# Optimization experiments

Hardware: AMD Instinct MI355X
Metric: run time of the kernel (lower is better)

Reference implementation:

```python
import jax, jax.numpy as jnp
import numpy as np

N_NODES = 100000
N_EDGES = 1600000
F_IN, F_HID, F_OUT = 64, 64, 32


def setup_inputs() -> dict:
    key = jax.random.key(0)
    k1, k2, k3, k4 = jax.random.split(key, 4)
    x = jax.random.normal(k1, (N_NODES, F_IN), dtype=jnp.float32)
    edge_idx = jax.random.randint(k2, (2, N_EDGES), 0, N_NODES, dtype=jnp.int64)
    W1 = jax.random.normal(k3, (F_IN, F_HID), dtype=jnp.float32) * (1.0 / np.sqrt(F_IN))
    b1 = jnp.zeros((F_HID,), dtype=jnp.float32)
    W2 = jax.random.normal(k4, (F_HID, F_OUT), dtype=jnp.float32) * (1.0 / np.sqrt(F_HID))
    b2 = jnp.zeros((F_OUT,), dtype=jnp.float32)
    return {"x": x, "edge_idx": edge_idx, "W1": W1, "b1": b1, "W2": W2, "b2": b2}


def _gcn_conv(h, src, dst, norm, W, b, n):
    # PyG GCNConv: transform first, then normalized sum aggregation, then bias.
    h = h @ W                                   # [N, F_out]
    msg = h[src] * norm[:, None]                # [E+N, F_out] gather + scale
    agg = jax.ops.segment_sum(msg, dst, num_segments=n)  # scatter-add
    return agg + b


def reference(x, edge_idx, W1, b1, W2, b2):
    n = x.shape[0]
    loop = jnp.arange(n, dtype=edge_idx.dtype)
    src = jnp.concatenate([edge_idx[0], loop])  # add self-loops
    dst = jnp.concatenate([edge_idx[1], loop])
    # symmetric normalization D^-1/2 (A+I) D^-1/2
    deg = jax.ops.segment_sum(jnp.ones_like(dst, dtype=x.dtype), dst, num_segments=n)
    dinv = jnp.where(deg > 0, jax.lax.rsqrt(deg), 0.0)
    norm = dinv[src] * dinv[dst]                # [E+N]

    h = _gcn_conv(x, src, dst, norm, W1, b1, n)
    h = jax.nn.relu(h)
    # dropout(p=0.5) is identity in eval mode (deterministic reference)
    out = _gcn_conv(h, src, dst, norm, W2, b2, n)
    return out
```

## Files before the change

### kernel.cpp

```cpp
#include <hip/hip_runtime.h>
#include <hip/hip_bf16.h>
#include <hip/hip_fp16.h>


#define N_FEAT_IN 64
#define B2SHIFT 9
#define CHUNK 4096
#define CAP 12288
#define CSRCAP 20480

struct alignas(8) half4 { __half2 lo, hi; };
struct alignas(16) half8 { __half2 h[4]; };

__global__ __launch_bounds__(256) void init_k(int* __restrict__ gcur) {
    gcur[threadIdx.x] = 0;
}

__global__ __launch_bounds__(1024) void place_k(const int* __restrict__ src,
                                                const int* __restrict__ dst,
                                                int* __restrict__ gcur,
                                                unsigned* __restrict__ bedges, int E) {
    __shared__ int h[256];
    __shared__ int cur[256];
    int t = threadIdx.x;
    if (t < 256) h[t] = 0;
    __syncthreads();
    int base = blockIdx.x * CHUNK;
    int end = min(base + CHUNK, E);
    for (int i = base + t; i < end; i += 1024)
        atomicAdd(&h[dst[i] >> B2SHIFT], 1);
    __syncthreads();
    if (t < 256) {
        int cnt = h[t];
        int b0 = cnt ? atomicAdd(&gcur[t], cnt) : 0;
        cur[t] = t * CAP + b0;
    }
    __syncthreads();
    for (int i = base + t; i < end; i += 1024) {
        int d = dst[i];
        int p = atomicAdd(&cur[d >> B2SHIFT], 1);
        bedges[p] = ((unsigned)src[i] << B2SHIFT) | (unsigned)(d & 511);
    }
}

__global__ __launch_bounds__(1024) void bucket_csr(const int* __restrict__ gcnt,
                                                   const unsigned* __restrict__ bedges,
                                                   int* __restrict__ row_ptr,
                                                   int* __restrict__ rend,
                                                   float* __restrict__ dinv,
                                                   int* __restrict__ csr_src, int n) {
    __shared__ int lh[512];
    __shared__ int cur[512];
    int t = threadIdx.x;
    if (t < 512) lh[t] = 0;
    __syncthreads();
    int b = blockIdx.x;
    int beg = b * CAP;
    int end = beg + gcnt[b];
    for (int i = beg + t; i < end; i += 1024)
        atomicAdd(&lh[bedges[i] & 511], 1);
    __syncthreads();
    int c = (t < 512) ? lh[t] : 0;
    __syncthreads();
    int cp = (c + 15) & ~15;
    if (t < 512) lh[t] = cp;
    __syncthreads();
    for (int off = 1; off < 512; off <<= 1) {
        int a = (t < 512 && t >= off) ? lh[t - off] : 0;
        __syncthreads();
        if (t < 512) lh[t] += a;
        __syncthreads();
    }
    int pb = b * CSRCAP;
    if (t < 512) {
        int d = (b << B2SHIFT) + t;
        int rbeg = pb + lh[t] - cp;
        cur[t] = rbeg;
        if (d < n) {
            row_ptr[d] = rbeg;
            rend[d] = rbeg + cp;
            dinv[d] = rsqrtf((float)c + 1.0f);
            for (int i = c; i < cp; ++i) csr_src[rbeg + i] = n;
        }
    }
    __syncthreads();
    for (int i = beg + t; i < end; i += 1024) {
        unsigned v = bedges[i];
        int p = atomicAdd(&cur[v & 511], 1);
        csr_src[p] = (int)(v >> B2SHIFT);
    }
}

__global__ __launch_bounds__(256) void gemm64(const float* __restrict__ A,
                                              const float* __restrict__ W,
                                              const float* __restrict__ dinv,
                                              __half* __restrict__ outh, int n) {
    __shared__ float AsT[64][132];
    __shared__ float Ws[64][64];

    const int t = threadIdx.x;
    const int r0 = blockIdx.x * 128;

    if (blockIdx.x == 0 && t < 64)
        outh[(size_t)n * 64 + t] = __float2half(0.f);

    for (int i = t; i < 64 * 16; i += 256) {
        int k = i >> 4;
        int c4 = (i & 15) * 4;
        *(float4*)&Ws[k][c4] = *(const float4*)&W[k * 64 + c4];
    }
    for (int i = t; i < 128 * 16; i += 256) {
        int row = i >> 4;
        int c4 = (i & 15) * 4;
        int g = r0 + row;
        float4 v = make_float4(0.f, 0.f, 0.f, 0.f);
        if (g < n) v = *(const float4*)&A[(size_t)g * 64 + c4];
        AsT[c4 + 0][row] = v.x;
        AsT[c4 + 1][row] = v.y;
        AsT[c4 + 2][row] = v.z;
        AsT[c4 + 3][row] = v.w;
    }
    __syncthreads();

    const int rg = t >> 3;
    const int cg = t & 7;
    float acc[4][8];
#pragma unroll
    for (int r = 0; r < 4; ++r)
#pragma unroll
        for (int j = 0; j < 8; ++j) acc[r][j] = 0.f;

#pragma unroll 4
    for (int k = 0; k < 64; ++k) {
        float4 a = *(const float4*)&AsT[k][rg * 4];
        float4 w0 = *(const float4*)&Ws[k][cg * 8];
        float4 w1 = *(const float4*)&Ws[k][cg * 8 + 4];
        float av[4] = {a.x, a.y, a.z, a.w};
        float wv[8] = {w0.x, w0.y, w0.z, w0.w, w1.x, w1.y, w1.z, w1.w};
#pragma unroll
        for (int r = 0; r < 4; ++r)
#pragma unroll
            for (int j = 0; j < 8; ++j)
                acc[r][j] = fmaf(av[r], wv[j], acc[r][j]);
    }

#pragma unroll
    for (int r = 0; r < 4; ++r) {
        int g = r0 + rg * 4 + r;
        if (g < n) {
            float sc = dinv[g];
            half8 h;
            h.h[0] = __floats2half2_rn(acc[r][0] * sc, acc[r][1] * sc);
            h.h[1] = __floats2half2_rn(acc[r][2] * sc, acc[r][3] * sc);
            h.h[2] = __floats2half2_rn(acc[r][4] * sc, acc[r][5] * sc);
            h.h[3] = __floats2half2_rn(acc[r][6] * sc, acc[r][7] * sc);
            *(half8*)&outh[(size_t)g * 64 + cg * 8] = h;
        }
    }
}

#define ACC8(v)                                                       \
    {                                                                 \
        float2 f0 = __half22float2((v).h[0]);                         \
        float2 f1 = __half22float2((v).h[1]);                         \
        float2 f2 = __half22float2((v).h[2]);                         \
        float2 f3 = __half22float2((v).h[3]);                         \
        a0 += f0.x; a1 += f0.y; a2 += f1.x; a3 += f1.y;               \
        a4 += f2.x; a5 += f2.y; a6 += f3.x; a7 += f3.y;               \
    }

#define AGG_LOOP16(STRIDE)                                            \
    if (beg < end) {                                                  \
        int4 ia = *(const int4*)&csr_src[beg];                        \
        int4 ib = *(const int4*)&csr_src[beg + 4];                    \
        int4 ic = *(const int4*)&csr_src[beg + 8];                    \
        int4 id = *(const int4*)&csr_src[beg + 12];                   \
        int jb = beg;                                                 \
        for (;;) {                                                    \
            int jn = jb + 16;                                         \
            bool more = jn < end;                                     \
            int js = more ? jn : beg;                                 \
            int4 na = *(const int4*)&csr_src[js];                     \
            int4 nb = *(const int4*)&csr_src[js + 4];                 \
            int4 nc = *(const int4*)&csr_src[js + 8];                 \
            int4 nd = *(const int4*)&csr_src[js + 12];                \
            half8 v0  = xrow[(size_t)ia.x * STRIDE];                  \
            half8 v1  = xrow[(size_t)ia.y * STRIDE];                  \
            half8 v2  = xrow[(size_t)ia.z * STRIDE];                  \
            half8 v3  = xrow[(size_t)ia.w * STRIDE];                  \
            half8 v4  = xrow[(size_t)ib.x * STRIDE];                  \
            half8 v5  = xrow[(size_t)ib.y * STRIDE];                  \
            half8 v6  = xrow[(size_t)ib.z * STRIDE];                  \
            half8 v7  = xrow[(size_t)ib.w * STRIDE];                  \
            half8 v8  = xrow[(size_t)ic.x * STRIDE];                  \
            half8 v9  = xrow[(size_t)ic.y * STRIDE];                  \
            half8 v10 = xrow[(size_t)ic.z * STRIDE];                  \
            half8 v11 = xrow[(size_t)ic.w * STRIDE];                  \
            half8 v12 = xrow[(size_t)id.x * STRIDE];                  \
            half8 v13 = xrow[(size_t)id.y * STRIDE];                  \
            half8 v14 = xrow[(size_t)id.z * STRIDE];                  \
            half8 v15 = xrow[(size_t)id.w * STRIDE];                  \
            ACC8(v0);  ACC8(v1);  ACC8(v2);  ACC8(v3);                \
            ACC8(v4);  ACC8(v5);  ACC8(v6);  ACC8(v7);                \
            ACC8(v8);  ACC8(v9);  ACC8(v10); ACC8(v11);               \
            ACC8(v12); ACC8(v13); ACC8(v14); ACC8(v15);               \
            if (!more) break;                                         \
            jb = jn; ia = na; ib = nb; ic = nc; id = nd;              \
        }                                                             \
    }

__global__ __launch_bounds__(256, 4) void agg64(const int* __restrict__ row_ptr,
                                                const int* __restrict__ rend,
                                                const int* __restrict__ csr_src,
                                                const float* __restrict__ dinv,
                                                const __half* __restrict__ xs1,
                                                const float* __restrict__ b1,
                                                __half* __restrict__ th, int n) {
    int d = blockIdx.x * 32 + (threadIdx.x >> 3);
    if (d >= n) return;
    int c = threadIdx.x & 7;
    const half8* __restrict__ xrow = (const half8*)xs1 + c;

    half8 sv = xrow[(size_t)d * 8];
    float a0, a1, a2, a3, a4, a5, a6, a7;
    {
        float2 f0 = __half22float2(sv.h[0]), f1 = __half22float2(sv.h[1]);
        float2 f2 = __half22float2(sv.h[2]), f3 = __half22float2(sv.h[3]);
        a0 = f0.x; a1 = f0.y; a2 = f1.x; a3 = f1.y;
        a4 = f2.x; a5 = f2.y; a6 = f3.x; a7 = f3.y;
    }

    int beg = row_ptr[d];
    int end = rend[d];
    AGG_LOOP16(8)

    float di = dinv[d];
    float4 ba = *(const float4*)&b1[8 * c];
    float4 bb = *(const float4*)&b1[8 * c + 4];
    float t0 = fmaxf(fmaf(di, a0, ba.x), 0.f);
    float t1 = fmaxf(fmaf(di, a1, ba.y), 0.f);
    float t2 = fmaxf(fmaf(di, a2, ba.z), 0.f);
    float t3 = fmaxf(fmaf(di, a3, ba.w), 0.f);
    float t4 = fmaxf(fmaf(di, a4, bb.x), 0.f);
    float t5 = fmaxf(fmaf(di, a5, bb.y), 0.f);
    float t6 = fmaxf(fmaf(di, a6, bb.z), 0.f);
    float t7 = fmaxf(fmaf(di, a7, bb.w), 0.f);
    half8 o;
    o.h[0] = __floats2half2_rn(t0, t1);
    o.h[1] = __floats2half2_rn(t2, t3);
    o.h[2] = __floats2half2_rn(t4, t5);
    o.h[3] = __floats2half2_rn(t6, t7);
    *(half8*)&th[(size_t)d * 64 + 8 * c] = o;
}

__global__ __launch_bounds__(256) void gemm32h(const __half* __restrict__ Ah,
                                               const float* __restrict__ W,
                                               const float* __restrict__ dinv,
                                               __half* __restrict__ outh, int n) {
    __shared__ float AsT[64][260];
    __shared__ float Ws[64][32];

    const int t = threadIdx.x;
    const int r0 = blockIdx.x * 256;

    if (blockIdx.x == 0 && t < 32)
        outh[(size_t)n * 32 + t] = __float2half(0.f);

    for (int i = t; i < 64 * 8; i += 256) {
        int k = i >> 3;
        int c4 = (i & 7) * 4;
        *(float4*)&Ws[k][c4] = *(const float4*)&W[k * 32 + c4];
    }
    for (int i = t; i < 256 * 8; i += 256) {
        int row = i >> 3;
        int c8 = (i & 7) * 8;
        int g = r0 + row;
        if (g < n) {
            half8 hv = *(const half8*)&Ah[(size_t)g * 64 + c8];
            float2 f0 = __half22float2(hv.h[0]), f1 = __half22float2(hv.h[1]);
            float2 f2 = __half22float2(hv.h[2]), f3 = __half22float2(hv.h[3]);
            AsT[c8 + 0][row] = f0.x; AsT[c8 + 1][row] = f0.y;
            AsT[c8 + 2][row] = f1.x; AsT[c8 + 3][row] = f1.y;
            AsT[c8 + 4][row] = f2.x; AsT[c8 + 5][row] = f2.y;
            AsT[c8 + 6][row] = f3.x; AsT[c8 + 7][row] = f3.y;
        } else {
#pragma unroll
            for (int j = 0; j < 8; ++j) AsT[c8 + j][row] = 0.f;
        }
    }
    __syncthreads();

    const int rg = t >> 2;
    const int cg = t & 3;
    float acc[4][8];
#pragma unroll
    for (int r = 0; r < 4; ++r)
#pragma unroll
        for (int j = 0; j < 8; ++j) acc[r][j] = 0.f;

#pragma unroll 4
    for (int k = 0; k < 64; ++k) {
        float4 a = *(const float4*)&AsT[k][rg * 4];
        float4 w0 = *(const float4*)&Ws[k][cg * 8];
        float4 w1 = *(const float4*)&Ws[k][cg * 8 + 4];
        float av[4] = {a.x, a.y, a.z, a.w};
        float wv[8] = {w0.x, w0.y, w0.z, w0.w, w1.x, w1.y, w1.z, w1.w};
#pragma unroll
        for (int r = 0; r < 4; ++r)
#pragma unroll
            for (int j = 0; j < 8; ++j)
                acc[r][j] = fmaf(av[r], wv[j], acc[r][j]);
    }

#pragma unroll
    for (int r = 0; r < 4; ++r) {
        int g = r0 + rg * 4 + r;
        if (g < n) {
            float sc = dinv[g];
            half8 h;
            h.h[0] = __floats2half2_rn(acc[r][0] * sc, acc[r][1] * sc);
            h.h[1] = __floats2half2_rn(acc[r][2] * sc, acc[r][3] * sc);
            h.h[2] = __floats2half2_rn(acc[r][4] * sc, acc[r][5] * sc);
            h.h[3] = __floats2half2_rn(acc[r][6] * sc, acc[r][7] * sc);
            *(half8*)&outh[(size_t)g * 32 + cg * 8] = h;
        }
    }
}

__global__ __launch_bounds__(256, 4) void agg32(const int* __restrict__ row_ptr,
                                                const int* __restrict__ rend,
                                                const int* __restrict__ csr_src,
                                                const float* __restrict__ dinv,
                                                const __half* __restrict__ xs2,
                                                const float* __restrict__ b2,
                                                float* __restrict__ out, int n) {
    int d = blockIdx.x * 64 + (threadIdx.x >> 2);
    if (d >= n) return;
    int c = threadIdx.x & 3;
    const half8* __restrict__ xrow = (const half8*)xs2 + c;

    half8 sv = xrow[(size_t)d * 4];
    float a0, a1, a2, a3, a4, a5, a6, a7;
    {
        float2 f0 = __half22float2(sv.h[0]), f1 = __half22float2(sv.h[1]);
        float2 f2 = __half22float2(sv.h[2]), f3 = __half22float2(sv.h[3]);
        a0 = f0.x; a1 = f0.y; a2 = f1.x; a3 = f1.y;
        a4 = f2.x; a5 = f2.y; a6 = f3.x; a7 = f3.y;
    }

    int beg = row_ptr[d];
    int end = rend[d];
    AGG_LOOP16(4)

    float di = dinv[d];
    float4 ba = *(const float4*)&b2[8 * c];
    float4 bb = *(const float4*)&b2[8 * c + 4];
    float4 r0, r1;
    r0.x = fmaf(di, a0, ba.x);
    r0.y = fmaf(di, a1, ba.y);
    r0.z = fmaf(di, a2, ba.z);
    r0.w = fmaf(di, a3, ba.w);
    r1.x = fmaf(di, a4, bb.x);
    r1.y = fmaf(di, a5, bb.y);
    r1.z = fmaf(di, a6, bb.z);
    r1.w = fmaf(di, a7, bb.w);
    *(float4*)&out[(size_t)d * 32 + 8 * c] = r0;
    *(float4*)&out[(size_t)d * 32 + 8 * c + 4] = r1;
}

extern "C" void kernel_launch(void* const* d_in, const int* in_sizes, int n_in,
                              void* d_out, int out_size, void* d_ws, size_t ws_size,
                              hipStream_t stream) {
    const float* x  = (const float*)d_in[0];
    const int*   ei = (const int*)d_in[1];
    const float* W1 = (const float*)d_in[2];
    const float* b1 = (const float*)d_in[3];
    const float* W2 = (const float*)d_in[4];
    const float* b2 = (const float*)d_in[5];
    float* out = (float*)d_out;

    const int n = in_sizes[0] / N_FEAT_IN;
    const int E = in_sizes[1] / 2;
    const int* srcI = ei;
    const int* dstI = ei + E;

    const int NB = (n + 511) >> B2SHIFT;
    const int NR = (E + CHUNK - 1) / CHUNK;

    char* ws = (char*)d_ws;
    size_t off = 0;
    auto alloc = [&](size_t bytes) {
        void* p = ws + off;
        off += (bytes + 255) & ~(size_t)255;
        return p;
    };
    float*    dinv    = (float*)alloc((size_t)n * 4);
    int*      row_ptr = (int*)alloc((size_t)(n + 1) * 4);
    int*      rend    = (int*)alloc((size_t)n * 4);
    int*      gcur    = (int*)alloc((size_t)256 * 4);
    unsigned* bedges  = (unsigned*)alloc((size_t)NB * CAP * 4);
    int*      csr_src = (int*)alloc((size_t)NB * CSRCAP * 4);
    __half*   xs1     = (__half*)alloc((size_t)(n + 1) * 64 * 2);
    __half*   th      = (__half*)alloc((size_t)n * 64 * 2);
    __half*   xs2     = (__half*)alloc((size_t)(n + 1) * 32 * 2);

    init_k<<<1, 256, 0, stream>>>(gcur);
    place_k<<<NR, 1024, 0, stream>>>(srcI, dstI, gcur, bedges, E);
    bucket_csr<<<NB, 1024, 0, stream>>>(gcur, bedges, row_ptr, rend, dinv, csr_src, n);

    gemm64<<<(n + 127) / 128, 256, 0, stream>>>(x, W1, dinv, xs1, n);

    agg64<<<(n + 31) / 32, 256, 0, stream>>>(row_ptr, rend, csr_src, dinv, xs1, b1, th, n);

    gemm32h<<<(n + 255) / 256, 256, 0, stream>>>(th, W2, dinv, xs2, n);

    agg32<<<(n + 63) / 64, 256, 0, stream>>>(row_ptr, rend, csr_src, dinv, xs2, b2, out, n);
}
```

Before: 201.1 us.

## Build CSR via global degree histogram and fuse layer-1 aggregation with second GEMM

```diff
diff --git a/kernel.cpp b/kernel.cpp
--- a/kernel.cpp
+++ b/kernel.cpp
@@ -6,88 +6,58 @@
 #define N_FEAT_IN 64
 #define B2SHIFT 9
 #define CHUNK 4096
-#define CAP 12288
-#define CSRCAP 20480
+#define CSRCAP 16384
 
 struct alignas(8) half4 { __half2 lo, hi; };
 struct alignas(16) half8 { __half2 h[4]; };
 
-__global__ __launch_bounds__(256) void init_k(int* __restrict__ gcur) {
-    gcur[threadIdx.x] = 0;
-}
-
-__global__ __launch_bounds__(1024) void place_k(const int* __restrict__ src,
-                                                const int* __restrict__ dst,
-                                                int* __restrict__ gcur,
-                                                unsigned* __restrict__ bedges, int E) {
-    __shared__ int h[256];
-    __shared__ int cur[256];
-    int t = threadIdx.x;
-    if (t < 256) h[t] = 0;
-    __syncthreads();
+__global__ __launch_bounds__(1024) void deg_hist(const int* __restrict__ dst,
+                                                 int* __restrict__ deg, int E) {
     int base = blockIdx.x * CHUNK;
     int end = min(base + CHUNK, E);
-    for (int i = base + t; i < end; i += 1024)
-        atomicAdd(&h[dst[i] >> B2SHIFT], 1);
-    __syncthreads();
-    if (t < 256) {
-        int cnt = h[t];
-        int b0 = cnt ? atomicAdd(&gcur[t], cnt) : 0;
-        cur[t] = t * CAP + b0;
-    }
-    __syncthreads();
-    for (int i = base + t; i < end; i += 1024) {
-        int d = dst[i];
-        int p = atomicAdd(&cur[d >> B2SHIFT], 1);
-        bedges[p] = ((unsigned)src[i] << B2SHIFT) | (unsigned)(d & 511);
-    }
-}
-
-__global__ __launch_bounds__(1024) void bucket_csr(const int* __restrict__ gcnt,
-                                                   const unsigned* __restrict__ bedges,
-                                                   int* __restrict__ row_ptr,
-                                                   int* __restrict__ rend,
-                                                   float* __restrict__ dinv,
-                                                   int* __restrict__ csr_src, int n) {
+    for (int i = base + threadIdx.x; i < end; i += 1024)
+        atomicAdd(&deg[dst[i]], 1);
+}
+
+__global__ __launch_bounds__(512) void rowscan_k(const int* __restrict__ deg,
+                                                 int* __restrict__ row_ptr,
+                                                 int* __restrict__ rend,
+                                                 int* __restrict__ cursor,
+                                                 float* __restrict__ dinv,
+                                                 int* __restrict__ csr_src, int n) {
     __shared__ int lh[512];
-    __shared__ int cur[512];
     int t = threadIdx.x;
-    if (t < 512) lh[t] = 0;
-    __syncthreads();
     int b = blockIdx.x;
-    int beg = b * CAP;
-    int end = beg + gcnt[b];
-    for (int i = beg + t; i < end; i += 1024)
-        atomicAdd(&lh[bedges[i] & 511], 1);
-    __syncthreads();
-    int c = (t < 512) ? lh[t] : 0;
-    __syncthreads();
-    int cp = (c + 15) & ~15;
-    if (t < 512) lh[t] = cp;
+    int d = (b << B2SHIFT) + t;
+    int c = (d < n) ? deg[d] : 0;
+    int cp = (c + 7) & ~7;
+    lh[t] = cp;
     __syncthreads();
     for (int off = 1; off < 512; off <<= 1) {
-        int a = (t < 512 && t >= off) ? lh[t - off] : 0;
+        int a = (t >= off) ? lh[t - off] : 0;
         __syncthreads();
-        if (t < 512) lh[t] += a;
+        lh[t] += a;
         __syncthreads();
     }
-    int pb = b * CSRCAP;
-    if (t < 512) {
-        int d = (b << B2SHIFT) + t;
-        int rbeg = pb + lh[t] - cp;
-        cur[t] = rbeg;
-        if (d < n) {
-            row_ptr[d] = rbeg;
-            rend[d] = rbeg + cp;
-            dinv[d] = rsqrtf((float)c + 1.0f);
-            for (int i = c; i < cp; ++i) csr_src[rbeg + i] = n;
-        }
-    }
-    __syncthreads();
-    for (int i = beg + t; i < end; i += 1024) {
-        unsigned v = bedges[i];
-        int p = atomicAdd(&cur[v & 511], 1);
-        csr_src[p] = (int)(v >> B2SHIFT);
+    if (d < n) {
+        int rbeg = b * CSRCAP + lh[t] - cp;
+        row_ptr[d] = rbeg;
+        rend[d] = rbeg + cp;
+        cursor[d] = rbeg;
+        dinv[d] = rsqrtf((float)c + 1.0f);
+        for (int i = c; i < cp; ++i) csr_src[rbeg + i] = n;
+    }
+}
+
+__global__ __launch_bounds__(1024) void scatter_k(const int* __restrict__ src,
+                                                  const int* __restrict__ dst,
+                                                  int* __restrict__ cursor,
+                                                  int* __restrict__ csr_src, int E) {
+    int base = blockIdx.x * CHUNK;
+    int end = min(base + CHUNK, E);
+    for (int i = base + threadIdx.x; i < end; i += 1024) {
+        int p = atomicAdd(&cursor[dst[i]], 1);
+        csr_src[p] = src[i];
     }
 }
 
@@ -169,152 +139,115 @@
         a4 += f2.x; a5 += f2.y; a6 += f3.x; a7 += f3.y;               \
     }
 
-#define AGG_LOOP16(STRIDE)                                            \
+#define AGG_LOOP8(STRIDE)                                             \
     if (beg < end) {                                                  \
         int4 ia = *(const int4*)&csr_src[beg];                        \
         int4 ib = *(const int4*)&csr_src[beg + 4];                    \
-        int4 ic = *(const int4*)&csr_src[beg + 8];                    \
-        int4 id = *(const int4*)&csr_src[beg + 12];                   \
         int jb = beg;                                                 \
         for (;;) {                                                    \
-            int jn = jb + 16;                                         \
+            int jn = jb + 8;                                          \
             bool more = jn < end;                                     \
             int js = more ? jn : beg;                                 \
             int4 na = *(const int4*)&csr_src[js];                     \
             int4 nb = *(const int4*)&csr_src[js + 4];                 \
-            int4 nc = *(const int4*)&csr_src[js + 8];                 \
-            int4 nd = *(const int4*)&csr_src[js + 12];                \
-            half8 v0  = xrow[(size_t)ia.x * STRIDE];                  \
-            half8 v1  = xrow[(size_t)ia.y * STRIDE];                  \
-            half8 v2  = xrow[(size_t)ia.z * STRIDE];                  \
-            half8 v3  = xrow[(size_t)ia.w * STRIDE];                  \
-            half8 v4  = xrow[(size_t)ib.x * STRIDE];                  \
-            half8 v5  = xrow[(size_t)ib.y * STRIDE];                  \
-            half8 v6  = xrow[(size_t)ib.z * STRIDE];                  \
-            half8 v7  = xrow[(size_t)ib.w * STRIDE];                  \
-            half8 v8  = xrow[(size_t)ic.x * STRIDE];                  \
-            half8 v9  = xrow[(size_t)ic.y * STRIDE];                  \
-            half8 v10 = xrow[(size_t)ic.z * STRIDE];                  \
-            half8 v11 = xrow[(size_t)ic.w * STRIDE];                  \
-            half8 v12 = xrow[(size_t)id.x * STRIDE];                  \
-            half8 v13 = xrow[(size_t)id.y * STRIDE];                  \
-            half8 v14 = xrow[(size_t)id.z * STRIDE];                  \
-            half8 v15 = xrow[(size_t)id.w * STRIDE];                  \
-            ACC8(v0);  ACC8(v1);  ACC8(v2);  ACC8(v3);                \
-            ACC8(v4);  ACC8(v5);  ACC8(v6);  ACC8(v7);                \
-            ACC8(v8);  ACC8(v9);  ACC8(v10); ACC8(v11);               \
-            ACC8(v12); ACC8(v13); ACC8(v14); ACC8(v15);               \
+            half8 v0 = xrow[(size_t)ia.x * STRIDE];                   \
+            half8 v1 = xrow[(size_t)ia.y * STRIDE];                   \
+            half8 v2 = xrow[(size_t)ia.z * STRIDE];                   \
+            half8 v3 = xrow[(size_t)ia.w * STRIDE];                   \
+            half8 v4 = xrow[(size_t)ib.x * STRIDE];                   \
+            half8 v5 = xrow[(size_t)ib.y * STRIDE];                   \
+            half8 v6 = xrow[(size_t)ib.z * STRIDE];                   \
+            half8 v7 = xrow[(size_t)ib.w * STRIDE];                   \
+            ACC8(v0); ACC8(v1); ACC8(v2); ACC8(v3);                   \
+            ACC8(v4); ACC8(v5); ACC8(v6); ACC8(v7);                   \
             if (!more) break;                                         \
-            jb = jn; ia = na; ib = nb; ic = nc; id = nd;              \
+            jb = jn; ia = na; ib = nb;                                \
         }                                                             \
     }
 
-__global__ __launch_bounds__(256, 4) void agg64(const int* __restrict__ row_ptr,
-                                                const int* __restrict__ rend,
-                                                const int* __restrict__ csr_src,
-                                                const float* __restrict__ dinv,
-                                                const __half* __restrict__ xs1,
-                                                const float* __restrict__ b1,
-                                                __half* __restrict__ th, int n) {
-    int d = blockIdx.x * 32 + (threadIdx.x >> 3);
-    if (d >= n) return;
-    int c = threadIdx.x & 7;
-    const half8* __restrict__ xrow = (const half8*)xs1 + c;
-
-    half8 sv = xrow[(size_t)d * 8];
-    float a0, a1, a2, a3, a4, a5, a6, a7;
-    {
-        float2 f0 = __half22float2(sv.h[0]), f1 = __half22float2(sv.h[1]);
-        float2 f2 = __half22float2(sv.h[2]), f3 = __half22float2(sv.h[3]);
-        a0 = f0.x; a1 = f0.y; a2 = f1.x; a3 = f1.y;
-        a4 = f2.x; a5 = f2.y; a6 = f3.x; a7 = f3.y;
-    }
-
-    int beg = row_ptr[d];
-    int end = rend[d];
-    AGG_LOOP16(8)
-
-    float di = dinv[d];
-    float4 ba = *(const float4*)&b1[8 * c];
-    float4 bb = *(const float4*)&b1[8 * c + 4];
-    float t0 = fmaxf(fmaf(di, a0, ba.x), 0.f);
-    float t1 = fmaxf(fmaf(di, a1, ba.y), 0.f);
-    float t2 = fmaxf(fmaf(di, a2, ba.z), 0.f);
-    float t3 = fmaxf(fmaf(di, a3, ba.w), 0.f);
-    float t4 = fmaxf(fmaf(di, a4, bb.x), 0.f);
-    float t5 = fmaxf(fmaf(di, a5, bb.y), 0.f);
-    float t6 = fmaxf(fmaf(di, a6, bb.z), 0.f);
-    float t7 = fmaxf(fmaf(di, a7, bb.w), 0.f);
-    half8 o;
-    o.h[0] = __floats2half2_rn(t0, t1);
-    o.h[1] = __floats2half2_rn(t2, t3);
-    o.h[2] = __floats2half2_rn(t4, t5);
-    o.h[3] = __floats2half2_rn(t6, t7);
-    *(half8*)&th[(size_t)d * 64 + 8 * c] = o;
-}
-
-__global__ __launch_bounds__(256) void gemm32h(const __half* __restrict__ Ah,
-                                               const float* __restrict__ W,
-                                               const float* __restrict__ dinv,
-                                               __half* __restrict__ outh, int n) {
-    __shared__ float AsT[64][260];
+__global__ __launch_bounds__(256) void agg_gemm32(const int* __restrict__ row_ptr,
+                                                  const int* __restrict__ rend,
+                                                  const int* __restrict__ csr_src,
+                                                  const float* __restrict__ dinv,
+                                                  const __half* __restrict__ xs1,
+                                                  const float* __restrict__ b1,
+                                                  const float* __restrict__ W2,
+                                                  __half* __restrict__ xs2, int n) {
+    __shared__ __half AsT[64][140];
     __shared__ float Ws[64][32];
 
     const int t = threadIdx.x;
-    const int r0 = blockIdx.x * 256;
+    const int r0 = blockIdx.x * 128;
 
     if (blockIdx.x == 0 && t < 32)
-        outh[(size_t)n * 32 + t] = __float2half(0.f);
+        xs2[(size_t)n * 32 + t] = __float2half(0.f);
 
     for (int i = t; i < 64 * 8; i += 256) {
         int k = i >> 3;
         int c4 = (i & 7) * 4;
-        *(float4*)&Ws[k][c4] = *(const float4*)&W[k * 32 + c4];
-    }
-    for (int i = t; i < 256 * 8; i += 256) {
-        int row = i >> 3;
-        int c8 = (i & 7) * 8;
-        int g = r0 + row;
-        if (g < n) {
-            half8 hv = *(const half8*)&Ah[(size_t)g * 64 + c8];
-            float2 f0 = __half22float2(hv.h[0]), f1 = __half22float2(hv.h[1]);
-            float2 f2 = __half22float2(hv.h[2]), f3 = __half22float2(hv.h[3]);
-            AsT[c8 + 0][row] = f0.x; AsT[c8 + 1][row] = f0.y;
-            AsT[c8 + 2][row] = f1.x; AsT[c8 + 3][row] = f1.y;
-            AsT[c8 + 4][row] = f2.x; AsT[c8 + 5][row] = f2.y;
-            AsT[c8 + 6][row] = f3.x; AsT[c8 + 7][row] = f3.y;
-        } else {
-#pragma unroll
-            for (int j = 0; j < 8; ++j) AsT[c8 + j][row] = 0.f;
+        *(float4*)&Ws[k][c4] = *(const float4*)&W2[k * 32 + c4];
+    }
+
+    const int sr = t >> 3;
+    const int c = t & 7;
+    const half8* __restrict__ xrow = (const half8*)xs1 + c;
+    float4 ba = *(const float4*)&b1[8 * c];
+    float4 bb = *(const float4*)&b1[8 * c + 4];
+
+#pragma unroll
+    for (int sub = 0; sub < 4; ++sub) {
+        int row = sub * 32 + sr;
+        int d = r0 + row;
+        if (d < n) {
+            half8 sv = xrow[(size_t)d * 8];
+            float a0, a1, a2, a3, a4, a5, a6, a7;
+            {
+                float2 f0 = __half22float2(sv.h[0]), f1 = __half22float2(sv.h[1]);
+                float2 f2 = __half22float2(sv.h[2]), f3 = __half22float2(sv.h[3]);
+                a0 = f0.x; a1 = f0.y; a2 = f1.x; a3 = f1.y;
+                a4 = f2.x; a5 = f2.y; a6 = f3.x; a7 = f3.y;
+            }
+            int beg = row_ptr[d];
+            int end = rend[d];
+            AGG_LOOP8(8)
+            float di = dinv[d];
+            AsT[8 * c + 0][row] = __float2half(fmaxf(fmaf(di, a0, ba.x), 0.f));
+            AsT[8 * c + 1][row] = __float2half(fmaxf(fmaf(di, a1, ba.y), 0.f));
+            AsT[8 * c + 2][row] = __float2half(fmaxf(fmaf(di, a2, ba.z), 0.f));
+            AsT[8 * c + 3][row] = __float2half(fmaxf(fmaf(di, a3, ba.w), 0.f));
+            AsT[8 * c + 4][row] = __float2half(fmaxf(fmaf(di, a4, bb.x), 0.f));
+            AsT[8 * c + 5][row] = __float2half(fmaxf(fmaf(di, a5, bb.y), 0.f));
+            AsT[8 * c + 6][row] = __float2half(fmaxf(fmaf(di, a6, bb.z), 0.f));
+            AsT[8 * c + 7][row] = __float2half(fmaxf(fmaf(di, a7, bb.w), 0.f));
         }
     }
     __syncthreads();
 
     const int rg = t >> 2;
     const int cg = t & 3;
-    float acc[4][8];
-#pragma unroll
-    for (int r = 0; r < 4; ++r)
+    float acc[2][8];
+#pragma unroll
+    for (int r = 0; r < 2; ++r)
 #pragma unroll
         for (int j = 0; j < 8; ++j) acc[r][j] = 0.f;
 
 #pragma unroll 4
     for (int k = 0; k < 64; ++k) {
-        float4 a = *(const float4*)&AsT[k][rg * 4];
+        float2 af = __half22float2(*(const __half2*)&AsT[k][rg * 2]);
         float4 w0 = *(const float4*)&Ws[k][cg * 8];
         float4 w1 = *(const float4*)&Ws[k][cg * 8 + 4];
-        float av[4] = {a.x, a.y, a.z, a.w};
+        float av[2] = {af.x, af.y};
         float wv[8] = {w0.x, w0.y, w0.z, w0.w, w1.x, w1.y, w1.z, w1.w};
 #pragma unroll
-        for (int r = 0; r < 4; ++r)
+        for (int r = 0; r < 2; ++r)
 #pragma unroll
             for (int j = 0; j < 8; ++j)
                 acc[r][j] = fmaf(av[r], wv[j], acc[r][j]);
     }
 
 #pragma unroll
-    for (int r = 0; r < 4; ++r) {
-        int g = r0 + rg * 4 + r;
+    for (int r = 0; r < 2; ++r) {
+        int g = r0 + rg * 2 + r;
         if (g < n) {
             float sc = dinv[g];
             half8 h;
@@ -322,18 +255,18 @@
             h.h[1] = __floats2half2_rn(acc[r][2] * sc, acc[r][3] * sc);
             h.h[2] = __floats2half2_rn(acc[r][4] * sc, acc[r][5] * sc);
             h.h[3] = __floats2half2_rn(acc[r][6] * sc, acc[r][7] * sc);
-            *(half8*)&outh[(size_t)g * 32 + cg * 8] = h;
+            *(half8*)&xs2[(size_t)g * 32 + cg * 8] = h;
         }
     }
 }
 
-__global__ __launch_bounds__(256, 4) void agg32(const int* __restrict__ row_ptr,
-                                                const int* __restrict__ rend,
-                                                const int* __restrict__ csr_src,
-                                                const float* __restrict__ dinv,
-                                                const __half* __restrict__ xs2,
-                                                const float* __restrict__ b2,
-                                                float* __restrict__ out, int n) {
+__global__ __launch_bounds__(256) void agg32(const int* __restrict__ row_ptr,
+                                             const int* __restrict__ rend,
+                                             const int* __restrict__ csr_src,
+                                             const float* __restrict__ dinv,
+                                             const __half* __restrict__ xs2,
+                                             const float* __restrict__ b2,
+                                             float* __restrict__ out, int n) {
     int d = blockIdx.x * 64 + (threadIdx.x >> 2);
     if (d >= n) return;
     int c = threadIdx.x & 3;
@@ -350,7 +283,7 @@
 
     int beg = row_ptr[d];
     int end = rend[d];
-    AGG_LOOP16(4)
+    AGG_LOOP8(4)
 
     float di = dinv[d];
     float4 ba = *(const float4*)&b2[8 * c];
@@ -395,24 +328,23 @@
         return p;
     };
     float*    dinv    = (float*)alloc((size_t)n * 4);
-    int*      row_ptr = (int*)alloc((size_t)(n + 1) * 4);
+    int*      row_ptr = (int*)alloc((size_t)n * 4);
     int*      rend    = (int*)alloc((size_t)n * 4);
-    int*      gcur    = (int*)alloc((size_t)256 * 4);
-    unsigned* bedges  = (unsigned*)alloc((size_t)NB * CAP * 4);
+    int*      deg     = (int*)alloc((size_t)n * 4);
+    int*      cursor  = (int*)alloc((size_t)n * 4);
     int*      csr_src = (int*)alloc((size_t)NB * CSRCAP * 4);
     __half*   xs1     = (__half*)alloc((size_t)(n + 1) * 64 * 2);
-    __half*   th      = (__half*)alloc((size_t)n * 64 * 2);
     __half*   xs2     = (__half*)alloc((size_t)(n + 1) * 32 * 2);
 
-    init_k<<<1, 256, 0, stream>>>(gcur);
-    place_k<<<NR, 1024, 0, stream>>>(srcI, dstI, gcur, bedges, E);
-    bucket_csr<<<NB, 1024, 0, stream>>>(gcur, bedges, row_ptr, rend, dinv, csr_src, n);
+    hipMemsetAsync(deg, 0, (size_t)n * 4, stream);
+    deg_hist<<<NR, 1024, 0, stream>>>(dstI, deg, E);
+    rowscan_k<<<NB, 512, 0, stream>>>(deg, row_ptr, rend, cursor, dinv, csr_src, n);
+    scatter_k<<<NR, 1024, 0, stream>>>(srcI, dstI, cursor, csr_src, E);
 
     gemm64<<<(n + 127) / 128, 256, 0, stream>>>(x, W1, dinv, xs1, n);
 
-    agg64<<<(n + 31) / 32, 256, 0, stream>>>(row_ptr, rend, csr_src, dinv, xs1, b1, th, n);
-
-    gemm32h<<<(n + 255) / 256, 256, 0, stream>>>(th, W2, dinv, xs2, n);
+    agg_gemm32<<<(n + 127) / 128, 256, 0, stream>>>(row_ptr, rend, csr_src, dinv,
+                                                    xs1, b1, W2, xs2, n);
 
     agg32<<<(n + 63) / 64, 256, 0, stream>>>(row_ptr, rend, csr_src, dinv, xs2, b2, out, n);
 }
```

Result: slower. 343.2 us (+70.7%).
